# Performance work log

Measured on AMD Instinct MI355X. Metric: run time of the kernel, lower is better.

The kernel has to match this reference:

```python
import jax, jax.numpy as jnp
import numpy as np

D_MODEL = 1024
N_HEADS = 16
N_PHASE = 128
HEAD_DIM = D_MODEL // N_HEADS
PHASE_PER_HEAD = N_PHASE // N_HEADS
CONTENT_SCALE = 1.0 / np.sqrt(HEAD_DIM)
PHASE_SCALE = 1.0 / np.sqrt(PHASE_PER_HEAD)
LN_EPS = 1e-5


def create_position_phases(L, n_phase, base=10000.0):
    # RoPE-style: each freq repeated at even/odd indices (interleaved)
    inv_freq = 1.0 / base ** (jnp.arange(0, n_phase, 2, dtype=jnp.float32) / n_phase)
    pos = jnp.arange(L, dtype=jnp.float32)
    sinusoid = pos[:, None] * inv_freq[None, :]          # (L, n_phase//2)
    return jnp.repeat(sinusoid, 2, axis=1)               # (L, n_phase)


def setup_inputs() -> dict:
    key = jax.random.key(0)
    ks = jax.random.split(key, 12)
    B, L, D, P = 1, 2048, D_MODEL, N_PHASE
    s = 0.02
    return {
        'x_real': jax.random.normal(ks[0], (B, L, D), jnp.float32),
        'x_imag': jax.random.normal(ks[1], (B, L, D), jnp.float32),
        'Wq': jax.random.normal(ks[2], (D, D), jnp.float32) * s,
        'Wk': jax.random.normal(ks[3], (D, D), jnp.float32) * s,
        'Wv': jax.random.normal(ks[4], (D, D), jnp.float32) * s,
        'Wqp': jax.random.normal(ks[5], (D, P), jnp.float32) * s,
        'bqp': jax.random.uniform(ks[6], (P,), jnp.float32, -np.pi, np.pi),
        'Wkp': jax.random.normal(ks[7], (D, P), jnp.float32) * s,
        'bkp': jax.random.uniform(ks[8], (P,), jnp.float32, -np.pi, np.pi),
        'Wo': jax.random.normal(ks[9], (D, D), jnp.float32) * s,
        'alpha_logit': jnp.zeros((N_HEADS, 1, 1), jnp.float32),
        'ln_gamma': jnp.ones((D,), jnp.float32),
        'ln_beta': jnp.zeros((D,), jnp.float32),
    }


def _split_heads(x, B, L, H, hd):
    return x.reshape(B, L, H, hd).transpose(0, 2, 1, 3)  # (B,H,L,hd)


def reference(x_real, x_imag, Wq, Wk, Wv, Wqp, bqp, Wkp, bkp, Wo,
              alpha_logit, ln_gamma, ln_beta):
    B, L, D = x_real.shape
    H, hd, p = N_HEADS, HEAD_DIM, PHASE_PER_HEAD

    Q = _split_heads(x_real @ Wq, B, L, H, hd)
    K = _split_heads(x_real @ Wk, B, L, H, hd)
    V = _split_heads(x_real @ Wv, B, L, H, hd)
    content = jnp.einsum('bhqd,bhkd->bhqk', Q, K) * CONTENT_SCALE

    pos_phase = create_position_phases(L, N_PHASE)        # (L, P)
    Qt = _split_heads(x_imag @ Wqp + bqp + pos_phase, B, L, H, p)
    Kt = _split_heads(x_imag @ Wkp + bkp + pos_phase, B, L, H, p)
    phase = (jnp.einsum('bhqp,bhkp->bhqk', jnp.cos(Qt), jnp.cos(Kt))
             + jnp.einsum('bhqp,bhkp->bhqk', jnp.sin(Qt), jnp.sin(Kt))) * PHASE_SCALE

    alpha = jax.nn.sigmoid(alpha_logit)                   # (H,1,1) broadcasts over (B,H,L,L)
    scores = (1.0 - alpha) * content + alpha * phase

    causal = jnp.triu(jnp.ones((L, L), bool), 1)
    scores = jnp.where(causal, -jnp.inf, scores)
    attn = jax.nn.softmax(scores, axis=-1)

    out = jnp.einsum('bhqk,bhkd->bhqd', attn, V)
    out = out.transpose(0, 2, 1, 3).reshape(B, L, D) @ Wo

    h = x_real + out
    mu = jnp.mean(h, axis=-1, keepdims=True)
    var = jnp.var(h, axis=-1, keepdims=True)
    out_real = (h - mu) / jnp.sqrt(var + LN_EPS) * ln_gamma + ln_beta
    return out_real, x_imag
```

## Files before the change

### kernel.cpp

```cpp
#include <hip/hip_runtime.h>
#include <hip/hip_bf16.h>
#include <math.h>

#define L 2048
#define D 1024
#define NH 16
#define HD 64
#define P 128
#define HDE 96
#define CONTENT_SCALE 0.125f
#define PHASE_SCALE   0.35355339059327373f
#define KLS 104
#define VTS 72
#define PLS 72
#define NSPLIT 4

typedef short bf16x8 __attribute__((ext_vector_type(8)));
typedef float f32x4 __attribute__((ext_vector_type(4)));

__device__ inline ushort f2b(float x) {
    __hip_bfloat16 b = __float2bfloat16(x);
    return *(ushort*)&b;
}
__device__ inline float b2f(ushort u) {
    unsigned v = (unsigned)u << 16;
    union { unsigned u; float f; } c; c.u = v; return c.f;
}

__device__ inline void sincos_hw(float ang, float* sn, float* cs) {
    float rev = ang * 0.15915494309189535f;
    rev -= floorf(rev);
    *sn = __builtin_amdgcn_sinf(rev);
    *cs = __builtin_amdgcn_cosf(rev);
}

__device__ inline void gld_lds16(const void* g, void* l) {
    __builtin_amdgcn_global_load_lds(
        (const __attribute__((address_space(1))) unsigned int*)g,
        (__attribute__((address_space(3))) unsigned int*)l,
        16, 0, 0);
}

__global__ void prep_kernel(const float* __restrict__ xr, const float* __restrict__ xi,
                            ushort* __restrict__ xrb, ushort* __restrict__ xib,
                            const float* __restrict__ W0, const float* __restrict__ W1,
                            const float* __restrict__ W2, const float* __restrict__ W3,
                            const float* __restrict__ W4, const float* __restrict__ W5,
                            ushort* __restrict__ T0, ushort* __restrict__ T1,
                            ushort* __restrict__ T2, ushort* __restrict__ T3,
                            ushort* __restrict__ Tp,
                            ushort* __restrict__ Qe, ushort* __restrict__ Ke) {
    __shared__ float tile[32][33];
    const int b = blockIdx.x;
    const int tid = threadIdx.x;
    if (b < 4096) {
        const float4* src = (b >> 11) ? (const float4*)xi : (const float4*)xr;
        ushort4* dst = (b >> 11) ? (ushort4*)xib : (ushort4*)xrb;
        int i = ((b & 2047) << 8) + tid;
        float4 v = src[i];
        ushort4 o;
        o.x = f2b(v.x); o.y = f2b(v.y); o.z = f2b(v.z); o.w = f2b(v.w);
        dst[i] = o;
    } else if (b < 8448) {
        int w = b - 4096;
        const float* W; ushort* T; int ncols, n0, k0;
        if (w < 4096) {
            int z = w >> 10, t = w & 1023;
            n0 = (t & 31) * 32; k0 = (t >> 5) * 32; ncols = D;
            W = (z == 0) ? W0 : ((z == 1) ? W1 : ((z == 2) ? W2 : W3));
            T = (z == 0) ? T0 : ((z == 1) ? T1 : ((z == 2) ? T2 : T3));
        } else {
            int w2 = w - 4096;
            int z = w2 >> 7, t = w2 & 127;
            n0 = (t & 3) * 32; k0 = (t >> 2) * 32; ncols = P;
            W = z ? W5 : W4;
            T = Tp + (size_t)z * P * D;
        }
        int tx = tid & 31, ty = tid >> 5;
#pragma unroll
        for (int i = 0; i < 4; i++)
            tile[ty + i * 8][tx] = W[(size_t)(k0 + ty + i * 8) * ncols + n0 + tx];
        __syncthreads();
#pragma unroll
        for (int i = 0; i < 4; i++)
            T[(size_t)(n0 + ty + i * 8) * D + k0 + tx] = f2b(tile[tx][ty + i * 8]);
    } else {
        int i = (b - 8448) * 256 + tid;
        size_t base = (size_t)i * HDE + 80;
        uint4 z4 = make_uint4(0, 0, 0, 0);
        *(uint4*)(Qe + base) = z4;
        *(uint4*)(Qe + base + 8) = z4;
        *(uint4*)(Ke + base) = z4;
        *(uint4*)(Ke + base + 8) = z4;
    }
}

__launch_bounds__(256)
__global__ void qkv_gemm(const ushort* __restrict__ Ab, const ushort* __restrict__ xib,
                         const ushort* __restrict__ Wtq, const ushort* __restrict__ Wtk,
                         const ushort* __restrict__ Wtv, const ushort* __restrict__ Wtp,
                         ushort* __restrict__ Qe, ushort* __restrict__ Ke,
                         ushort* __restrict__ Ve, const float* __restrict__ alpha,
                         const float* __restrict__ bqp, const float* __restrict__ bkp) {
    const int z = blockIdx.z;
    if (z == 3 && blockIdx.x >= 2) return;
    const ushort* At = (z == 3) ? xib : Ab;
    const ushort* Bt = (z == 0) ? Wtq : ((z == 1) ? Wtk : ((z == 2) ? Wtv : Wtp));
    __shared__ ushort As[128 * 32];
    __shared__ ushort Bs[128 * 32];
    const int tid = threadIdx.x;
    const int wave = tid >> 6, lane = tid & 63, quad = lane >> 4, ln16 = lane & 15;
    const int wm = wave >> 1, wn = wave & 1;
    const int m0 = blockIdx.y * 128, n0 = blockIdx.x * 128;
    f32x4 acc[4][4];
#pragma unroll
    for (int i = 0; i < 4; i++)
#pragma unroll
        for (int j = 0; j < 4; j++) acc[i][j] = (f32x4){0.f, 0.f, 0.f, 0.f};
    for (int kt = 0; kt < D; kt += 32) {
        __syncthreads();
#pragma unroll
        for (int i = 0; i < 2; i++) {
            int idx = i * 256 + tid;
            int row = idx >> 2, c8 = idx & 3;
            gld_lds16(At + (size_t)(m0 + row) * D + kt + c8 * 8, &As[idx * 8]);
            gld_lds16(Bt + (size_t)(n0 + row) * D + kt + c8 * 8, &Bs[idx * 8]);
        }
        __syncthreads();
        bf16x8 af[4], bfr[4];
#pragma unroll
        for (int t = 0; t < 4; t++) {
            af[t]  = *(const bf16x8*)(&As[(wm * 64 + t * 16 + ln16) * 32 + quad * 8]);
            bfr[t] = *(const bf16x8*)(&Bs[(wn * 64 + t * 16 + ln16) * 32 + quad * 8]);
        }
#pragma unroll
        for (int i = 0; i < 4; i++)
#pragma unroll
            for (int j = 0; j < 4; j++)
                acc[i][j] = __builtin_amdgcn_mfma_f32_16x16x32_bf16(af[i], bfr[j], acc[i][j], 0, 0, 0);
    }
    if (z < 3) {
        int hn = (n0 + wn * 64) >> 6;
        float s = 1.f;
        if (z == 0) s = (1.f - 1.f / (1.f + __expf(-alpha[hn]))) * CONTENT_SCALE;
        ushort* dst; int stride;
        if (z == 0)      { dst = Qe; stride = HDE; }
        else if (z == 1) { dst = Ke; stride = HDE; }
        else             { dst = Ve; stride = HD; }
#pragma unroll
        for (int i = 0; i < 4; i++)
#pragma unroll
            for (int j = 0; j < 4; j++) {
                int dcol = j * 16 + ln16;
#pragma unroll
                for (int r = 0; r < 4; r++) {
                    int m = m0 + wm * 64 + i * 16 + quad * 4 + r;
                    dst[((size_t)hn * L + m) * stride + dcol] = f2b(acc[i][j][r] * s);
                }
            }
    } else {
#pragma unroll
        for (int j = 0; j < 4; j++) {
            int cg = n0 + wn * 64 + j * 16 + ln16;
            int isQ = cg < P;
            int c = cg & (P - 1);
            int hh = c >> 3, jj = c & 7;
            float b = isQ ? bqp[c] : bkp[c];
            float sc = isQ ? (1.f / (1.f + __expf(-alpha[hh]))) * PHASE_SCALE : 1.f;
            float invf = __expf(-((float)(c & ~1) / 128.f) * 9.210340371976184f);
            ushort* dst = isQ ? Qe : Ke;
#pragma unroll
            for (int i = 0; i < 4; i++)
#pragma unroll
                for (int r = 0; r < 4; r++) {
                    int m = m0 + wm * 64 + i * 16 + quad * 4 + r;
                    float qt = acc[i][j][r] + b + (float)m * invf;
                    float sn, cs;
                    sincos_hw(qt, &sn, &cs);
                    size_t base = ((size_t)hh * L + m) * HDE;
                    dst[base + 64 + jj] = f2b(sc * cs);
                    dst[base + 72 + jj] = f2b(sc * sn);
                }
        }
    }
}

__launch_bounds__(256)
__global__ void flash_attn(const ushort* __restrict__ Qe, const ushort* __restrict__ Ke,
                           const ushort* __restrict__ Ve,
                           ushort* __restrict__ Opart, float* __restrict__ ml) {
    const int b = blockIdx.x;
    const int xcd = b & 7;
    const int r5 = b >> 3;
    const int h = xcd * 2 + (r5 & 1);
    const int cA = (r5 >> 1) & 15, cB = 31 - cA;
    const int z = r5 >> 5;
    const int tid = threadIdx.x;
    const int wave = tid >> 6, lane = tid & 63, quad = lane >> 4, ln16 = lane & 15;
    const int nTA = cA + 1, nTB = cB + 1;
    const int sA = (z * nTA) >> 2, nA = (((z + 1) * nTA) >> 2) - sA;
    const int sB = (z * nTB) >> 2, nB = (((z + 1) * nTB) >> 2) - sB;
    const int ntot = nA + nB;

    ushort* Op = Opart + (size_t)z * L * D;
    float* mlp = ml + (size_t)z * NH * L;

    __shared__ ushort Kl[64 * KLS];
    __shared__ ushort Vt[HD * VTS];
    __shared__ ushort Pl[4][16 * PLS];

    const ushort* Kh  = Ke + (size_t)h * L * HDE;
    const ushort* Vh  = Ve + (size_t)h * L * HD;
    const ushort* Qh0 = Qe + (size_t)h * L * HDE;

    const int krow = tid & 63, dg = wave;

    bf16x8 onesv;
#pragma unroll
    for (int i = 0; i < 8; i++) onesv[i] = (short)0x3F80;

    if (nA == 0) {
        const int q0z = cA * 64 + wave * 16;
#pragma unroll
        for (int r = 0; r < 4; r++) {
            int q = q0z + quad * 4 + r;
            ushort* dst = Op + (size_t)q * D + h * HD;
#pragma unroll
            for (int nt = 0; nt < 4; nt++) dst[nt * 16 + ln16] = 0;
            if (ln16 == 0) mlp[(size_t)h * L + q] = 0.f;
        }
    }

    int t0 = (nA > 0) ? sA : sB;
    bf16x8 kreg[3], vreg[2];
    {
        const ushort* Ksrc = Kh + (size_t)(t0 * 64) * HDE;
#pragma unroll
        for (int ii = 0; ii < 3; ii++)
            kreg[ii] = *(const bf16x8*)(Ksrc + (size_t)(ii * 256 + tid) * 8);
#pragma unroll
        for (int i = 0; i < 2; i++)
            vreg[i] = *(const bf16x8*)(Vh + (size_t)(t0 * 64 + krow) * HD + dg * 16 + i * 8);
    }

    bf16x8 qa[3];
    f32x4 o[4], ol;

    for (int tt = 0; tt < ntot; tt++) {
        const int inB = (tt >= nA);
        const int c  = inB ? cB : cA;
        const int t  = inB ? sB + (tt - nA) : sA + tt;
        const int k0 = t * 64;
        const int q0 = c * 64 + wave * 16;

        __syncthreads();
#pragma unroll
        for (int ii = 0; ii < 3; ii++) {
            int idx = ii * 256 + tid;
            int row = idx / 12, c12 = idx - row * 12;
            *(bf16x8*)(&Kl[row * KLS + c12 * 8]) = kreg[ii];
        }
#pragma unroll
        for (int i = 0; i < 2; i++)
#pragma unroll
            for (int jj = 0; jj < 8; jj++)
                Vt[(dg * 16 + i * 8 + jj) * VTS + krow] = (ushort)vreg[i][jj];
        __syncthreads();

        if (tt + 1 < ntot) {
            int inB2 = (tt + 1 >= nA);
            int t2 = inB2 ? sB + (tt + 1 - nA) : sA + tt + 1;
            int k02 = t2 * 64;
            const ushort* Ksrc = Kh + (size_t)k02 * HDE;
#pragma unroll
            for (int ii = 0; ii < 3; ii++)
                kreg[ii] = *(const bf16x8*)(Ksrc + (size_t)(ii * 256 + tid) * 8);
#pragma unroll
            for (int i = 0; i < 2; i++)
                vreg[i] = *(const bf16x8*)(Vh + (size_t)(k02 + krow) * HD + dg * 16 + i * 8);
        }

        if (tt == 0 || tt == nA) {
            const ushort* Qh = Qh0 + (size_t)q0 * HDE;
#pragma unroll
            for (int kc = 0; kc < 3; kc++)
                qa[kc] = *(const bf16x8*)(Qh + (size_t)ln16 * HDE + kc * 32 + quad * 8);
#pragma unroll
            for (int nt = 0; nt < 4; nt++) o[nt] = (f32x4){0.f, 0.f, 0.f, 0.f};
            ol = (f32x4){0.f, 0.f, 0.f, 0.f};
        }

        f32x4 s[4];
#pragma unroll
        for (int st = 0; st < 4; st++) s[st] = (f32x4){0.f, 0.f, 0.f, 0.f};
#pragma unroll
        for (int kc = 0; kc < 3; kc++)
#pragma unroll
            for (int st = 0; st < 4; st++) {
                bf16x8 kb = *(const bf16x8*)(&Kl[(st * 16 + ln16) * KLS + kc * 32 + quad * 8]);
                s[st] = __builtin_amdgcn_mfma_f32_16x16x32_bf16(qa[kc], kb, s[st], 0, 0, 0);
            }
        if (t == c) {
#pragma unroll
            for (int st = 0; st < 4; st++) {
                int key = k0 + st * 16 + ln16;
#pragma unroll
                for (int r = 0; r < 4; r++)
                    if (key > q0 + quad * 4 + r) s[st][r] = -1e30f;
            }
        }
#pragma unroll
        for (int st = 0; st < 4; st++)
#pragma unroll
            for (int r = 0; r < 4; r++)
                Pl[wave][(quad * 4 + r) * PLS + st * 16 + ln16] = f2b(__expf(s[st][r]));
        bf16x8 pa0 = *(const bf16x8*)(&Pl[wave][ln16 * PLS + quad * 8]);
        bf16x8 pa1 = *(const bf16x8*)(&Pl[wave][ln16 * PLS + 32 + quad * 8]);
#pragma unroll
        for (int nt = 0; nt < 4; nt++) {
            bf16x8 vb0 = *(const bf16x8*)(&Vt[(nt * 16 + ln16) * VTS + quad * 8]);
            bf16x8 vb1 = *(const bf16x8*)(&Vt[(nt * 16 + ln16) * VTS + 32 + quad * 8]);
            o[nt] = __builtin_amdgcn_mfma_f32_16x16x32_bf16(pa0, vb0, o[nt], 0, 0, 0);
            o[nt] = __builtin_amdgcn_mfma_f32_16x16x32_bf16(pa1, vb1, o[nt], 0, 0, 0);
        }
        ol = __builtin_amdgcn_mfma_f32_16x16x32_bf16(pa0, onesv, ol, 0, 0, 0);
        ol = __builtin_amdgcn_mfma_f32_16x16x32_bf16(pa1, onesv, ol, 0, 0, 0);

        if (tt == nA - 1 || tt == ntot - 1) {
#pragma unroll
            for (int r = 0; r < 4; r++) {
                int q = q0 + quad * 4 + r;
                ushort* dst = Op + (size_t)q * D + h * HD;
#pragma unroll
                for (int nt = 0; nt < 4; nt++)
                    dst[nt * 16 + ln16] = f2b(o[nt][r]);
                if (ln16 == 0) mlp[(size_t)h * L + q] = ol[r];
            }
        }
    }
}

__global__ void comb_kernel(const ushort* __restrict__ Opart, const float* __restrict__ ml,
                            ushort* __restrict__ AOb) {
    int q = blockIdx.x;
    int t = threadIdx.x;
    int h = t >> 4;
    float lsum = 0.f;
#pragma unroll
    for (int zz = 0; zz < NSPLIT; zz++)
        lsum += ml[(size_t)zz * NH * L + (size_t)h * L + q];
    float inv = 1.f / lsum;
    size_t idx = (size_t)q * D + t * 4;
    float ox = 0.f, oy = 0.f, oz = 0.f, ow = 0.f;
#pragma unroll
    for (int zz = 0; zz < NSPLIT; zz++) {
        ushort4 a = *(const ushort4*)(Opart + (size_t)zz * L * D + idx);
        ox += b2f(a.x); oy += b2f(a.y); oz += b2f(a.z); ow += b2f(a.w);
    }
    ushort4 o;
    o.x = f2b(ox * inv); o.y = f2b(oy * inv);
    o.z = f2b(oz * inv); o.w = f2b(ow * inv);
    *(ushort4*)(AOb + idx) = o;
}

__launch_bounds__(256)
__global__ void wo_gemm(const ushort* __restrict__ Ab, const ushort* __restrict__ Bt,
                        float* __restrict__ C) {
    __shared__ ushort As[128 * 32];
    __shared__ ushort Bs[128 * 32];
    const int tid = threadIdx.x;
    const int wave = tid >> 6, lane = tid & 63, quad = lane >> 4, ln16 = lane & 15;
    const int wm = wave >> 1, wn = wave & 1;
    const int m0 = blockIdx.y * 128, n0 = blockIdx.x * 128;
    f32x4 acc[4][4];
#pragma unroll
    for (int i = 0; i < 4; i++)
#pragma unroll
        for (int j = 0; j < 4; j++) acc[i][j] = (f32x4){0.f, 0.f, 0.f, 0.f};
    for (int kt = 0; kt < D; kt += 32) {
        __syncthreads();
#pragma unroll
        for (int i = 0; i < 2; i++) {
            int idx = i * 256 + tid;
            int row = idx >> 2, c8 = idx & 3;
            gld_lds16(Ab + (size_t)(m0 + row) * D + kt + c8 * 8, &As[idx * 8]);
            gld_lds16(Bt + (size_t)(n0 + row) * D + kt + c8 * 8, &Bs[idx * 8]);
        }
        __syncthreads();
        bf16x8 af[4], bfr[4];
#pragma unroll
        for (int t = 0; t < 4; t++) {
            af[t]  = *(const bf16x8*)(&As[(wm * 64 + t * 16 + ln16) * 32 + quad * 8]);
            bfr[t] = *(const bf16x8*)(&Bs[(wn * 64 + t * 16 + ln16) * 32 + quad * 8]);
        }
#pragma unroll
        for (int i = 0; i < 4; i++)
#pragma unroll
            for (int j = 0; j < 4; j++)
                acc[i][j] = __builtin_amdgcn_mfma_f32_16x16x32_bf16(af[i], bfr[j], acc[i][j], 0, 0, 0);
    }
#pragma unroll
    for (int i = 0; i < 4; i++)
#pragma unroll
        for (int j = 0; j < 4; j++)
#pragma unroll
            for (int r = 0; r < 4; r++) {
                int m = m0 + wm * 64 + i * 16 + quad * 4 + r;
                int n = n0 + wn * 64 + j * 16 + ln16;
                C[(size_t)m * D + n] = acc[i][j][r];
            }
}

__global__ void ln_kernel(const float* __restrict__ xr, const float* __restrict__ o2,
                          const float* __restrict__ gamma, const float* __restrict__ beta,
                          float* __restrict__ outp, const float4* __restrict__ xi4,
                          float4* __restrict__ out1) {
    int l = blockIdx.x;
    int tid = threadIdx.x;
    int wave = tid >> 6;
    __shared__ float red[8];
    float hv[4];
    float s = 0.f;
#pragma unroll
    for (int i = 0; i < 4; i++) {
        int c = tid + i * 256;
        hv[i] = xr[(size_t)l * D + c] + o2[(size_t)l * D + c];
        s += hv[i];
    }
    out1[(size_t)l * (D / 4) + tid] = xi4[(size_t)l * (D / 4) + tid];
#pragma unroll
    for (int off = 1; off < 64; off <<= 1) s += __shfl_xor(s, off);
    if ((tid & 63) == 0) red[wave] = s;
    __syncthreads();
    float mu = (red[0] + red[1] + red[2] + red[3]) * (1.f / D);
    float v = 0.f;
#pragma unroll
    for (int i = 0; i < 4; i++) { float d = hv[i] - mu; v += d * d; }
#pragma unroll
    for (int off = 1; off < 64; off <<= 1) v += __shfl_xor(v, off);
    __syncthreads();
    if ((tid & 63) == 0) red[4 + wave] = v;
    __syncthreads();
    float rstd = rsqrtf((red[4] + red[5] + red[6] + red[7]) * (1.f / D) + 1e-5f);
#pragma unroll
    for (int i = 0; i < 4; i++) {
        int c = tid + i * 256;
        outp[(size_t)l * D + c] = (hv[i] - mu) * rstd * gamma[c] + beta[c];
    }
}

extern "C" void kernel_launch(void* const* d_in, const int* in_sizes, int n_in,
                              void* d_out, int out_size, void* d_ws, size_t ws_size,
                              hipStream_t stream) {
    const float* xr    = (const float*)d_in[0];
    const float* xi    = (const float*)d_in[1];
    const float* Wq    = (const float*)d_in[2];
    const float* Wk    = (const float*)d_in[3];
    const float* Wv    = (const float*)d_in[4];
    const float* Wqp   = (const float*)d_in[5];
    const float* bqp   = (const float*)d_in[6];
    const float* Wkp   = (const float*)d_in[7];
    const float* bkp   = (const float*)d_in[8];
    const float* Wo    = (const float*)d_in[9];
    const float* alpha = (const float*)d_in[10];
    const float* gamma = (const float*)d_in[11];
    const float* beta  = (const float*)d_in[12];

    const size_t LD = (size_t)L * D;
    const size_t MB = 1024 * 1024;

    char* A8 = (char*)d_out;
    char* B8 = A8 + LD * 4;
    ushort* xib = (ushort*)A8;
    ushort* AOb = (ushort*)A8;
    ushort* Wot = (ushort*)(A8 + 4 * MB);
    ushort* Wtq = (ushort*)(A8 + 6 * MB);
    ushort* xrb = (ushort*)B8;
    ushort* Wtk = (ushort*)(B8 + 4 * MB);
    ushort* Wtv = (ushort*)(B8 + 6 * MB);
    float* outf = (float*)d_out;

    ushort* Qe = (ushort*)d_ws;
    ushort* Ke = Qe + (size_t)NH * L * HDE;
    ushort* Ve = Ke + (size_t)NH * L * HDE;
    ushort* Wqpkt = Ve + (size_t)NH * L * HD;
    ushort* Opart = Wqpkt + (size_t)256 * D;
    float*  mlbuf = (float*)(Opart + (size_t)NSPLIT * LD);
    float*  O2 = (float*)d_ws;

    prep_kernel<<<8576, 256, 0, stream>>>(xr, xi, xrb, xib,
                                          Wq, Wk, Wv, Wo, Wqp, Wkp,
                                          Wtq, Wtk, Wtv, Wot, Wqpkt, Qe, Ke);

    qkv_gemm<<<dim3(8, 16, 4), 256, 0, stream>>>(xrb, xib, Wtq, Wtk, Wtv, Wqpkt,
                                                 Qe, Ke, Ve, alpha, bqp, bkp);

    flash_attn<<<1024, 256, 0, stream>>>(Qe, Ke, Ve, Opart, mlbuf);

    comb_kernel<<<L, 256, 0, stream>>>(Opart, mlbuf, AOb);

    wo_gemm<<<dim3(8, 16), 256, 0, stream>>>(AOb, Wot, O2);

    ln_kernel<<<L, 256, 0, stream>>>(xr, O2, gamma, beta, outf,
                                     (const float4*)xi, (float4*)(B8));
}
```

Before: 200.0 us.

## Stream K/V fragments from global memory and give each wave 32 query rows

The projection kernel now writes V transposed (head, dim, seq) with packed 4-element stores, so the attention kernel can load V fragments straight from global memory. The flash attention kernel drops the shared-memory K/V staging, both block barriers and the register prefetch. Each wave now owns 32 query rows of one chunk (waves 0-1 take chunk A, waves 2-3 take chunk B) and reads K/V fragments directly, with s_setprio set around the MFMA sections. This removes LDS traffic and synchronisation, but every wave re-reads K/V from global memory or cache, and the two wave pairs now do unequal amounts of work.

```diff
diff --git a/kernel.cpp b/kernel.cpp
--- a/kernel.cpp
+++ b/kernel.cpp
@@ -10,8 +10,6 @@
 #define HDE 96
 #define CONTENT_SCALE 0.125f
 #define PHASE_SCALE   0.35355339059327373f
-#define KLS 104
-#define VTS 72
 #define PLS 72
 #define NSPLIT 4
 
@@ -139,14 +137,23 @@
             for (int j = 0; j < 4; j++)
                 acc[i][j] = __builtin_amdgcn_mfma_f32_16x16x32_bf16(af[i], bfr[j], acc[i][j], 0, 0, 0);
     }
-    if (z < 3) {
+    if (z == 2) {
         int hn = (n0 + wn * 64) >> 6;
-        float s = 1.f;
-        if (z == 0) s = (1.f - 1.f / (1.f + __expf(-alpha[hn]))) * CONTENT_SCALE;
-        ushort* dst; int stride;
-        if (z == 0)      { dst = Qe; stride = HDE; }
-        else if (z == 1) { dst = Ke; stride = HDE; }
-        else             { dst = Ve; stride = HD; }
+#pragma unroll
+        for (int i = 0; i < 4; i++)
+#pragma unroll
+            for (int j = 0; j < 4; j++) {
+                int d = j * 16 + ln16;
+                int m = m0 + wm * 64 + i * 16 + quad * 4;
+                ushort4 pk;
+                pk.x = f2b(acc[i][j][0]); pk.y = f2b(acc[i][j][1]);
+                pk.z = f2b(acc[i][j][2]); pk.w = f2b(acc[i][j][3]);
+                *(ushort4*)(Ve + ((size_t)hn * HD + d) * L + m) = pk;
+            }
+    } else if (z < 2) {
+        int hn = (n0 + wn * 64) >> 6;
+        float s = (z == 0) ? (1.f - 1.f / (1.f + __expf(-alpha[hn]))) * CONTENT_SCALE : 1.f;
+        ushort* dst = (z == 0) ? Qe : Ke;
 #pragma unroll
         for (int i = 0; i < 4; i++)
 #pragma unroll
@@ -155,7 +162,7 @@
 #pragma unroll
                 for (int r = 0; r < 4; r++) {
                     int m = m0 + wm * 64 + i * 16 + quad * 4 + r;
-                    dst[((size_t)hn * L + m) * stride + dcol] = f2b(acc[i][j][r] * s);
+                    dst[((size_t)hn * L + m) * HDE + dcol] = f2b(acc[i][j][r] * s);
                 }
             }
     } else {
@@ -187,7 +194,7 @@
 
 __launch_bounds__(256)
 __global__ void flash_attn(const ushort* __restrict__ Qe, const ushort* __restrict__ Ke,
-                           const ushort* __restrict__ Ve,
+                           const ushort* __restrict__ Vte,
                            ushort* __restrict__ Opart, float* __restrict__ ml) {
     const int b = blockIdx.x;
     const int xcd = b & 7;
@@ -197,147 +204,139 @@
     const int z = r5 >> 5;
     const int tid = threadIdx.x;
     const int wave = tid >> 6, lane = tid & 63, quad = lane >> 4, ln16 = lane & 15;
-    const int nTA = cA + 1, nTB = cB + 1;
-    const int sA = (z * nTA) >> 2, nA = (((z + 1) * nTA) >> 2) - sA;
-    const int sB = (z * nTB) >> 2, nB = (((z + 1) * nTB) >> 2) - sB;
-    const int ntot = nA + nB;
+
+    const int c = (wave < 2) ? cA : cB;
+    const int wsub = wave & 1;
+    const int nT_all = c + 1;
+    const int s0 = (z * nT_all) >> 2;
+    const int nT = (((z + 1) * nT_all) >> 2) - s0;
 
     ushort* Op = Opart + (size_t)z * L * D;
     float* mlp = ml + (size_t)z * NH * L;
 
-    __shared__ ushort Kl[64 * KLS];
-    __shared__ ushort Vt[HD * VTS];
-    __shared__ ushort Pl[4][16 * PLS];
-
-    const ushort* Kh  = Ke + (size_t)h * L * HDE;
-    const ushort* Vh  = Ve + (size_t)h * L * HD;
-    const ushort* Qh0 = Qe + (size_t)h * L * HDE;
-
-    const int krow = tid & 63, dg = wave;
+    __shared__ ushort Pl[4][32 * PLS];
+
+    const ushort* Kh = Ke + (size_t)h * L * HDE;
+    const ushort* Vh = Vte + (size_t)h * HD * L;
+    const ushort* Qh = Qe + (size_t)h * L * HDE;
+
+    const int q0 = c * 64 + wsub * 32;
+
+    if (nT == 0) {
+#pragma unroll
+        for (int u = 0; u < 2; u++)
+#pragma unroll
+            for (int r = 0; r < 4; r++) {
+                int q = q0 + u * 16 + quad * 4 + r;
+                ushort* dst = Op + (size_t)q * D + h * HD;
+#pragma unroll
+                for (int nt = 0; nt < 4; nt++) dst[nt * 16 + ln16] = 0;
+                if (ln16 == 0) mlp[(size_t)h * L + q] = 0.f;
+            }
+        return;
+    }
 
     bf16x8 onesv;
 #pragma unroll
     for (int i = 0; i < 8; i++) onesv[i] = (short)0x3F80;
 
-    if (nA == 0) {
-        const int q0z = cA * 64 + wave * 16;
+    bf16x8 qa[2][3];
+#pragma unroll
+    for (int u = 0; u < 2; u++)
+#pragma unroll
+        for (int kc = 0; kc < 3; kc++)
+            qa[u][kc] = *(const bf16x8*)(Qh + (size_t)(q0 + u * 16 + ln16) * HDE + kc * 32 + quad * 8);
+
+    f32x4 o[2][4], ol[2];
+#pragma unroll
+    for (int u = 0; u < 2; u++) {
+#pragma unroll
+        for (int nt = 0; nt < 4; nt++) o[u][nt] = (f32x4){0.f, 0.f, 0.f, 0.f};
+        ol[u] = (f32x4){0.f, 0.f, 0.f, 0.f};
+    }
+
+    for (int t = s0; t < s0 + nT; t++) {
+        const int k0 = t * 64;
+
+        f32x4 s[2][4];
+#pragma unroll
+        for (int u = 0; u < 2; u++)
+#pragma unroll
+            for (int st = 0; st < 4; st++) s[u][st] = (f32x4){0.f, 0.f, 0.f, 0.f};
+
+        __builtin_amdgcn_s_setprio(1);
+#pragma unroll
+        for (int st = 0; st < 4; st++) {
+            const ushort* Krow = Kh + (size_t)(k0 + st * 16 + ln16) * HDE + quad * 8;
+            bf16x8 kb0 = *(const bf16x8*)(Krow);
+            bf16x8 kb1 = *(const bf16x8*)(Krow + 32);
+            bf16x8 kb2 = *(const bf16x8*)(Krow + 64);
+#pragma unroll
+            for (int u = 0; u < 2; u++) {
+                s[u][st] = __builtin_amdgcn_mfma_f32_16x16x32_bf16(qa[u][0], kb0, s[u][st], 0, 0, 0);
+                s[u][st] = __builtin_amdgcn_mfma_f32_16x16x32_bf16(qa[u][1], kb1, s[u][st], 0, 0, 0);
+                s[u][st] = __builtin_amdgcn_mfma_f32_16x16x32_bf16(qa[u][2], kb2, s[u][st], 0, 0, 0);
+            }
+        }
+        __builtin_amdgcn_s_setprio(0);
+
+        if (t == c) {
+#pragma unroll
+            for (int u = 0; u < 2; u++)
+#pragma unroll
+                for (int st = 0; st < 4; st++) {
+                    int key = k0 + st * 16 + ln16;
+#pragma unroll
+                    for (int r = 0; r < 4; r++)
+                        if (key > q0 + u * 16 + quad * 4 + r) s[u][st][r] = -1e30f;
+                }
+        }
+#pragma unroll
+        for (int u = 0; u < 2; u++)
+#pragma unroll
+            for (int st = 0; st < 4; st++)
+#pragma unroll
+                for (int r = 0; r < 4; r++)
+                    Pl[wave][(u * 16 + quad * 4 + r) * PLS + st * 16 + ln16] = f2b(__expf(s[u][st][r]));
+
+        bf16x8 pa[2][2];
+#pragma unroll
+        for (int u = 0; u < 2; u++) {
+            pa[u][0] = *(const bf16x8*)(&Pl[wave][(u * 16 + ln16) * PLS + quad * 8]);
+            pa[u][1] = *(const bf16x8*)(&Pl[wave][(u * 16 + ln16) * PLS + 32 + quad * 8]);
+        }
+
+        __builtin_amdgcn_s_setprio(1);
+#pragma unroll
+        for (int nt = 0; nt < 4; nt++) {
+            const ushort* Vrow = Vh + (size_t)(nt * 16 + ln16) * L + k0 + quad * 8;
+            bf16x8 vb0 = *(const bf16x8*)(Vrow);
+            bf16x8 vb1 = *(const bf16x8*)(Vrow + 32);
+#pragma unroll
+            for (int u = 0; u < 2; u++) {
+                o[u][nt] = __builtin_amdgcn_mfma_f32_16x16x32_bf16(pa[u][0], vb0, o[u][nt], 0, 0, 0);
+                o[u][nt] = __builtin_amdgcn_mfma_f32_16x16x32_bf16(pa[u][1], vb1, o[u][nt], 0, 0, 0);
+            }
+        }
+#pragma unroll
+        for (int u = 0; u < 2; u++) {
+            ol[u] = __builtin_amdgcn_mfma_f32_16x16x32_bf16(pa[u][0], onesv, ol[u], 0, 0, 0);
+            ol[u] = __builtin_amdgcn_mfma_f32_16x16x32_bf16(pa[u][1], onesv, ol[u], 0, 0, 0);
+        }
+        __builtin_amdgcn_s_setprio(0);
+    }
+
+#pragma unroll
+    for (int u = 0; u < 2; u++)
 #pragma unroll
         for (int r = 0; r < 4; r++) {
-            int q = q0z + quad * 4 + r;
+            int q = q0 + u * 16 + quad * 4 + r;
             ushort* dst = Op + (size_t)q * D + h * HD;
 #pragma unroll
-            for (int nt = 0; nt < 4; nt++) dst[nt * 16 + ln16] = 0;
-            if (ln16 == 0) mlp[(size_t)h * L + q] = 0.f;
-        }
-    }
-
-    int t0 = (nA > 0) ? sA : sB;
-    bf16x8 kreg[3], vreg[2];
-    {
-        const ushort* Ksrc = Kh + (size_t)(t0 * 64) * HDE;
-#pragma unroll
-        for (int ii = 0; ii < 3; ii++)
-            kreg[ii] = *(const bf16x8*)(Ksrc + (size_t)(ii * 256 + tid) * 8);
-#pragma unroll
-        for (int i = 0; i < 2; i++)
-            vreg[i] = *(const bf16x8*)(Vh + (size_t)(t0 * 64 + krow) * HD + dg * 16 + i * 8);
-    }
-
-    bf16x8 qa[3];
-    f32x4 o[4], ol;
-
-    for (int tt = 0; tt < ntot; tt++) {
-        const int inB = (tt >= nA);
-        const int c  = inB ? cB : cA;
-        const int t  = inB ? sB + (tt - nA) : sA + tt;
-        const int k0 = t * 64;
-        const int q0 = c * 64 + wave * 16;
-
-        __syncthreads();
-#pragma unroll
-        for (int ii = 0; ii < 3; ii++) {
-            int idx = ii * 256 + tid;
-            int row = idx / 12, c12 = idx - row * 12;
-            *(bf16x8*)(&Kl[row * KLS + c12 * 8]) = kreg[ii];
-        }
-#pragma unroll
-        for (int i = 0; i < 2; i++)
-#pragma unroll
-            for (int jj = 0; jj < 8; jj++)
-                Vt[(dg * 16 + i * 8 + jj) * VTS + krow] = (ushort)vreg[i][jj];
-        __syncthreads();
-
-        if (tt + 1 < ntot) {
-            int inB2 = (tt + 1 >= nA);
-            int t2 = inB2 ? sB + (tt + 1 - nA) : sA + tt + 1;
-            int k02 = t2 * 64;
-            const ushort* Ksrc = Kh + (size_t)k02 * HDE;
-#pragma unroll
-            for (int ii = 0; ii < 3; ii++)
-                kreg[ii] = *(const bf16x8*)(Ksrc + (size_t)(ii * 256 + tid) * 8);
-#pragma unroll
-            for (int i = 0; i < 2; i++)
-                vreg[i] = *(const bf16x8*)(Vh + (size_t)(k02 + krow) * HD + dg * 16 + i * 8);
-        }
-
-        if (tt == 0 || tt == nA) {
-            const ushort* Qh = Qh0 + (size_t)q0 * HDE;
-#pragma unroll
-            for (int kc = 0; kc < 3; kc++)
-                qa[kc] = *(const bf16x8*)(Qh + (size_t)ln16 * HDE + kc * 32 + quad * 8);
-#pragma unroll
-            for (int nt = 0; nt < 4; nt++) o[nt] = (f32x4){0.f, 0.f, 0.f, 0.f};
-            ol = (f32x4){0.f, 0.f, 0.f, 0.f};
-        }
-
-        f32x4 s[4];
-#pragma unroll
-        for (int st = 0; st < 4; st++) s[st] = (f32x4){0.f, 0.f, 0.f, 0.f};
-#pragma unroll
-        for (int kc = 0; kc < 3; kc++)
-#pragma unroll
-            for (int st = 0; st < 4; st++) {
-                bf16x8 kb = *(const bf16x8*)(&Kl[(st * 16 + ln16) * KLS + kc * 32 + quad * 8]);
-                s[st] = __builtin_amdgcn_mfma_f32_16x16x32_bf16(qa[kc], kb, s[st], 0, 0, 0);
-            }
-        if (t == c) {
-#pragma unroll
-            for (int st = 0; st < 4; st++) {
-                int key = k0 + st * 16 + ln16;
-#pragma unroll
-                for (int r = 0; r < 4; r++)
-                    if (key > q0 + quad * 4 + r) s[st][r] = -1e30f;
-            }
-        }
-#pragma unroll
-        for (int st = 0; st < 4; st++)
-#pragma unroll
-            for (int r = 0; r < 4; r++)
-                Pl[wave][(quad * 4 + r) * PLS + st * 16 + ln16] = f2b(__expf(s[st][r]));
-        bf16x8 pa0 = *(const bf16x8*)(&Pl[wave][ln16 * PLS + quad * 8]);
-        bf16x8 pa1 = *(const bf16x8*)(&Pl[wave][ln16 * PLS + 32 + quad * 8]);
-#pragma unroll
-        for (int nt = 0; nt < 4; nt++) {
-            bf16x8 vb0 = *(const bf16x8*)(&Vt[(nt * 16 + ln16) * VTS + quad * 8]);
-            bf16x8 vb1 = *(const bf16x8*)(&Vt[(nt * 16 + ln16) * VTS + 32 + quad * 8]);
-            o[nt] = __builtin_amdgcn_mfma_f32_16x16x32_bf16(pa0, vb0, o[nt], 0, 0, 0);
-            o[nt] = __builtin_amdgcn_mfma_f32_16x16x32_bf16(pa1, vb1, o[nt], 0, 0, 0);
-        }
-        ol = __builtin_amdgcn_mfma_f32_16x16x32_bf16(pa0, onesv, ol, 0, 0, 0);
-        ol = __builtin_amdgcn_mfma_f32_16x16x32_bf16(pa1, onesv, ol, 0, 0, 0);
-
-        if (tt == nA - 1 || tt == ntot - 1) {
-#pragma unroll
-            for (int r = 0; r < 4; r++) {
-                int q = q0 + quad * 4 + r;
-                ushort* dst = Op + (size_t)q * D + h * HD;
-#pragma unroll
-                for (int nt = 0; nt < 4; nt++)
-                    dst[nt * 16 + ln16] = f2b(o[nt][r]);
-                if (ln16 == 0) mlp[(size_t)h * L + q] = ol[r];
-            }
-        }
-    }
+            for (int nt = 0; nt < 4; nt++)
+                dst[nt * 16 + ln16] = f2b(o[u][nt][r]);
+            if (ln16 == 0) mlp[(size_t)h * L + q] = ol[u][r];
+        }
 }
 
 __global__ void comb_kernel(const ushort* __restrict__ Opart, const float* __restrict__ ml,
```

Measured after the change: 227.5 us. +13.8%, slower.
